# Optimization experiments

Measured on AMD Instinct MI355X. Metric: run time of the kernel, lower is better.

Reference implementation:

```python
import jax, jax.numpy as jnp
import numpy as np

NODE_DIM = 512
HIDDEN = 4096
N_NODES = 4096  # must equal HIDDEN for pool Linear to typecheck (as in source)
N_EDGES = 131072


def setup_inputs() -> dict:
    key = jax.random.key(0)
    ks = jax.random.split(key, 12)
    s1 = 0.02
    x = jax.random.normal(ks[0], (N_NODES, NODE_DIM), dtype=jnp.float32)
    edge_index = jax.random.randint(ks[1], (2, N_EDGES), 0, N_NODES, dtype=jnp.int64)
    # encoder: Linear(node_dim, hidden) -> ReLU -> Linear(hidden, hidden)
    W1 = jax.random.normal(ks[2], (NODE_DIM, HIDDEN), dtype=jnp.float32) * s1
    b1 = jnp.zeros((HIDDEN,), dtype=jnp.float32)
    W2 = jax.random.normal(ks[3], (HIDDEN, HIDDEN), dtype=jnp.float32) * s1
    b2 = jnp.zeros((HIDDEN,), dtype=jnp.float32)
    # pool: Linear(hidden, hidden) -> ReLU -> Linear(hidden, 1)
    W3 = jax.random.normal(ks[4], (HIDDEN, HIDDEN), dtype=jnp.float32) * s1
    b3 = jnp.zeros((HIDDEN,), dtype=jnp.float32)
    W4 = jax.random.normal(ks[5], (HIDDEN, 1), dtype=jnp.float32) * s1
    b4 = jnp.zeros((1,), dtype=jnp.float32)
    return {"x": x, "edge_index": edge_index, "W1": W1, "b1": b1,
            "W2": W2, "b2": b2, "W3": W3, "b3": b3, "W4": W4, "b4": b4}


def reference(x, edge_index, W1, b1, W2, b2, W3, b3, W4, b4):
    # encoder MLP: [N, node_dim] -> [N, hidden]
    h = jax.nn.relu(x @ W1 + b1) @ W2 + b2
    # kernel_vector = (h @ h.T).sum(1) == h @ h.sum(0)  (avoids O(N^2) Gram)
    s = h.sum(axis=0)                 # [hidden]
    kernel_vector = h @ s             # [N]
    kv = kernel_vector[None, :]       # [1, N] with N == hidden
    pooled = jax.nn.relu(kv @ W3 + b3) @ W4 + b4   # [1, 1]
    return pooled
```

## Files before the change

kernel.cpp:

```cpp
#include <hip/hip_runtime.h>

#define NODES 4096
#define NDIM  512
#define HID   4096

typedef __attribute__((ext_vector_type(8))) short bf16x8;
typedef __attribute__((ext_vector_type(4))) float f32x4;

__device__ __forceinline__ float b2f(short v) {
  union { unsigned int u; float f; } c;
  c.u = ((unsigned int)(unsigned short)v) << 16;
  return c.f;
}
__device__ __forceinline__ short f2b(float f) {
  union { float f; unsigned int u; } c; c.f = f;
  unsigned int r = c.u + 0x7fffu + ((c.u >> 16) & 1u);
  return (short)(r >> 16);
}

__global__ __launch_bounds__(256) void k_prep(const float* __restrict__ x,
                                              const float* __restrict__ W1,
                                              const float* __restrict__ b2,
                                              const float* __restrict__ b3,
                                              short* __restrict__ xb,
                                              short* __restrict__ w1t,
                                              float* __restrict__ aacc,
                                              float* __restrict__ svec,
                                              float* __restrict__ uacc) {
  __shared__ float tile[32][33];
  int b = blockIdx.x;
  if (b < 2048) {
    int i = (b * 256 + threadIdx.x) * 4;
    float4 v = *(const float4*)(x + i);
    short4 o;
    o.x = f2b(v.x); o.y = f2b(v.y); o.z = f2b(v.z); o.w = f2b(v.w);
    *(short4*)(xb + i) = o;
  } else if (b < 4096) {
    int t = b - 2048;
    int n0 = (t & 127) * 32;
    int k0 = (t >> 7) * 32;
    int tx = threadIdx.x & 31, ty = threadIdx.x >> 5;
    #pragma unroll
    for (int j = 0; j < 4; ++j) {
      int kk = ty + j * 8;
      tile[kk][tx] = W1[(size_t)(k0 + kk) * HID + n0 + tx];
    }
    __syncthreads();
    #pragma unroll
    for (int j = 0; j < 4; ++j) {
      int nn = ty + j * 8;
      w1t[(size_t)(n0 + nn) * NDIM + k0 + tx] = f2b(tile[tx][nn]);
    }
  } else {
    int j = (b - 4096) * 256 + threadIdx.x;
    aacc[j] = 0.0f;
    svec[j] = (float)NODES * b2[j];
    uacc[j] = b3[j];
  }
}

__global__ __launch_bounds__(512, 2) void k_gemm1(const short* __restrict__ xb,
                                                  const short* __restrict__ w1t,
                                                  const float* __restrict__ b1,
                                                  short* __restrict__ Aout,
                                                  float* __restrict__ colsum) {
  extern __shared__ char smem[];
  __shared__ float csum[256];

  const int tid  = threadIdx.x;
  const int lane = tid & 63;
  const int wid  = tid >> 6;
  const int wr   = wid >> 2;
  const int wc   = wid & 3;

  int bswz = (blockIdx.x & 7) * 32 + (blockIdx.x >> 3);
  const int brow = (bswz >> 4) * 256, bcol = (bswz & 15) * 256;

  f32x4 acc[8][4];
  #pragma unroll
  for (int i = 0; i < 8; ++i)
    #pragma unroll
    for (int j = 0; j < 4; ++j)
      acc[i][j] = (f32x4){0.f, 0.f, 0.f, 0.f};

  if (tid < 256) csum[tid] = 0.f;

  const int fr = lane & 15;
  const int fk = (lane >> 4) * 8;

  const int off0 = tid * 16;
  const int row0 = off0 >> 6, ce0 = (off0 & 63) >> 1;
  const short* gA0 = xb  + (size_t)(brow + row0) * NDIM + ce0;
  const short* gA1 = xb  + (size_t)(brow + row0 + 128) * NDIM + ce0;
  const short* gB0 = w1t + (size_t)(bcol + row0) * NDIM + ce0;
  const short* gB1 = w1t + (size_t)(bcol + row0 + 128) * NDIM + ce0;

  auto STAGE = [&](int buf, int kt2) {
    char* baseA = smem + buf * 32768;
    char* baseB = smem + 65536 + buf * 32768;
    const int ks = kt2 * 64;
    #pragma unroll
    for (int kh = 0; kh < 2; ++kh) {
      __builtin_amdgcn_global_load_lds(
          (const __attribute__((address_space(1))) void*)(gA0 + ks + kh * 32),
          (__attribute__((address_space(3))) void*)(baseA + kh * 16384 + off0), 16, 0, 0);
      __builtin_amdgcn_global_load_lds(
          (const __attribute__((address_space(1))) void*)(gA1 + ks + kh * 32),
          (__attribute__((address_space(3))) void*)(baseA + kh * 16384 + off0 + 8192), 16, 0, 0);
      __builtin_amdgcn_global_load_lds(
          (const __attribute__((address_space(1))) void*)(gB0 + ks + kh * 32),
          (__attribute__((address_space(3))) void*)(baseB + kh * 16384 + off0), 16, 0, 0);
      __builtin_amdgcn_global_load_lds(
          (const __attribute__((address_space(1))) void*)(gB1 + ks + kh * 32),
          (__attribute__((address_space(3))) void*)(baseB + kh * 16384 + off0 + 8192), 16, 0, 0);
    }
  };

  auto COMPUTE = [&](int buf) {
    #pragma unroll
    for (int kh = 0; kh < 2; ++kh) {
      bf16x8 af[8], bfr[4];
      const short* Ab = (const short*)(smem + buf * 32768 + kh * 16384);
      const short* Bb = (const short*)(smem + 65536 + buf * 32768 + kh * 16384);
      #pragma unroll
      for (int ni = 0; ni < 4; ++ni)
        bfr[ni] = *(const bf16x8*)(Bb + (wc * 64 + ni * 16 + fr) * 32 + fk);
      #pragma unroll
      for (int mi = 0; mi < 8; ++mi)
        af[mi] = *(const bf16x8*)(Ab + (wr * 128 + mi * 16 + fr) * 32 + fk);
      __builtin_amdgcn_s_setprio(1);
      #pragma unroll
      for (int mi = 0; mi < 8; ++mi)
        #pragma unroll
        for (int ni = 0; ni < 4; ++ni)
          acc[mi][ni] = __builtin_amdgcn_mfma_f32_16x16x32_bf16(bfr[ni], af[mi],
                                                                acc[mi][ni], 0, 0, 0);
      __builtin_amdgcn_s_setprio(0);
    }
  };

  STAGE(0, 0);
  #pragma unroll 1
  for (int kt2 = 0; kt2 < NDIM / 64 - 1; ++kt2) {
    STAGE((kt2 + 1) & 1, kt2 + 1);
    asm volatile("s_waitcnt vmcnt(8)" ::: "memory");
    __builtin_amdgcn_s_barrier();
    COMPUTE(kt2 & 1);
    __builtin_amdgcn_s_barrier();
  }
  asm volatile("s_waitcnt vmcnt(0)" ::: "memory");
  __builtin_amdgcn_s_barrier();
  COMPUTE((NDIM / 64 - 1) & 1);

  const int cr = lane & 15;
  const int cg = (lane >> 4) * 4;
  float4 bias4[4];
  #pragma unroll
  for (int ni = 0; ni < 4; ++ni)
    bias4[ni] = *(const float4*)(b1 + bcol + wc * 64 + ni * 16 + cg);

  float cl[4][4];
  #pragma unroll
  for (int ni = 0; ni < 4; ++ni)
    #pragma unroll
    for (int r = 0; r < 4; ++r)
      cl[ni][r] = 0.f;

  #pragma unroll
  for (int mi = 0; mi < 8; ++mi) {
    int grow = brow + wr * 128 + mi * 16 + cr;
    short* orow = Aout + (size_t)grow * HID + bcol + wc * 64;
    #pragma unroll
    for (int ni = 0; ni < 4; ++ni) {
      float v0 = fmaxf(acc[mi][ni][0] + bias4[ni].x, 0.f);
      float v1 = fmaxf(acc[mi][ni][1] + bias4[ni].y, 0.f);
      float v2 = fmaxf(acc[mi][ni][2] + bias4[ni].z, 0.f);
      float v3 = fmaxf(acc[mi][ni][3] + bias4[ni].w, 0.f);
      cl[ni][0] += v0; cl[ni][1] += v1; cl[ni][2] += v2; cl[ni][3] += v3;
      short4 o;
      o.x = f2b(v0); o.y = f2b(v1); o.z = f2b(v2); o.w = f2b(v3);
      *(short4*)(orow + ni * 16 + cg) = o;
    }
  }
  #pragma unroll
  for (int ni = 0; ni < 4; ++ni)
    #pragma unroll
    for (int r = 0; r < 4; ++r) {
      #pragma unroll
      for (int m = 1; m < 16; m <<= 1)
        cl[ni][r] += __shfl_xor(cl[ni][r], m);
    }
  if (cr == 0) {
    #pragma unroll
    for (int ni = 0; ni < 4; ++ni)
      #pragma unroll
      for (int r = 0; r < 4; ++r)
        atomicAdd(&csum[wc * 64 + ni * 16 + cg + r], cl[ni][r]);
  }
  __syncthreads();
  if (tid < 256) atomicAdd(&colsum[bcol + tid], csum[tid]);
}

__global__ __launch_bounds__(256) void k_gemv_at(const float* __restrict__ W,
                                                 const float* __restrict__ vin,
                                                 float* __restrict__ vout) {
  const int col = blockIdx.x * 1024 + threadIdx.x * 4;
  const int r0  = blockIdx.y * 64;
  float4 accv = {0.f, 0.f, 0.f, 0.f};
  const float* base = W + (size_t)r0 * HID + col;
  #pragma unroll 16
  for (int i = 0; i < 64; ++i) {
    float vi = vin[r0 + i];
    float4 wv = *(const float4*)(base + (size_t)i * HID);
    accv.x += vi * wv.x; accv.y += vi * wv.y;
    accv.z += vi * wv.z; accv.w += vi * wv.w;
  }
  atomicAdd(&vout[col + 0], accv.x);
  atomicAdd(&vout[col + 1], accv.y);
  atomicAdd(&vout[col + 2], accv.z);
  atomicAdd(&vout[col + 3], accv.w);
}

__global__ __launch_bounds__(256) void k_gemv_row(const float* __restrict__ W,
                                                  const float* __restrict__ vin,
                                                  const float* __restrict__ b2,
                                                  float* __restrict__ vout,
                                                  float* __restrict__ beta) {
  __shared__ float red[4];
  if (blockIdx.x == HID / 4) {
    float p = 0.f;
    for (int j = threadIdx.x; j < HID; j += 256) p += b2[j] * vin[j];
    #pragma unroll
    for (int o = 32; o > 0; o >>= 1) p += __shfl_down(p, o);
    int lane = threadIdx.x & 63, w = threadIdx.x >> 6;
    if (lane == 0) red[w] = p;
    __syncthreads();
    if (threadIdx.x == 0) beta[0] = red[0] + red[1] + red[2] + red[3];
    return;
  }
  int w = threadIdx.x >> 6, lane = threadIdx.x & 63;
  int row = blockIdx.x * 4 + w;
  const float* base = W + (size_t)row * HID;
  float p = 0.f;
  #pragma unroll 8
  for (int j = lane * 4; j < HID; j += 256) {
    float4 wv = *(const float4*)(base + j);
    float4 sv = *(const float4*)(vin + j);
    p += wv.x * sv.x + wv.y * sv.y + wv.z * sv.z + wv.w * sv.w;
  }
  #pragma unroll
  for (int o = 32; o > 0; o >>= 1) p += __shfl_down(p, o);
  if (lane == 0) vout[row] = p;
}

__global__ __launch_bounds__(256) void k_kv(const short* __restrict__ A,
                                            const float* __restrict__ t,
                                            const float* __restrict__ beta,
                                            float* __restrict__ kv) {
  int w = threadIdx.x >> 6, lane = threadIdx.x & 63;
  int row = blockIdx.x * 4 + w;
  const short* base = A + (size_t)row * HID;
  float p = 0.f;
  #pragma unroll
  for (int j = lane * 8; j < HID; j += 512) {
    bf16x8 av = *(const bf16x8*)(base + j);
    float4 t0 = *(const float4*)(t + j);
    float4 t1 = *(const float4*)(t + j + 4);
    p += b2f(av[0]) * t0.x + b2f(av[1]) * t0.y + b2f(av[2]) * t0.z + b2f(av[3]) * t0.w
       + b2f(av[4]) * t1.x + b2f(av[5]) * t1.y + b2f(av[6]) * t1.z + b2f(av[7]) * t1.w;
  }
  #pragma unroll
  for (int o = 32; o > 0; o >>= 1) p += __shfl_down(p, o);
  if (lane == 0) kv[row] = p + beta[0];
}

__global__ __launch_bounds__(256) void k_final(const float* __restrict__ uacc,
                                               const float* __restrict__ W4,
                                               const float* __restrict__ b4,
                                               float* __restrict__ out) {
  __shared__ float red[4];
  float p = 0.f;
  for (int j = threadIdx.x; j < HID; j += 256) {
    float uv = uacc[j];
    uv = uv > 0.f ? uv : 0.f;
    p += uv * W4[j];
  }
  #pragma unroll
  for (int o = 32; o > 0; o >>= 1) p += __shfl_down(p, o);
  int lane = threadIdx.x & 63, w = threadIdx.x >> 6;
  if (lane == 0) red[w] = p;
  __syncthreads();
  if (threadIdx.x == 0) out[0] = red[0] + red[1] + red[2] + red[3] + b4[0];
}

extern "C" void kernel_launch(void* const* d_in, const int* in_sizes, int n_in,
                              void* d_out, int out_size, void* d_ws, size_t ws_size,
                              hipStream_t stream) {
  const float* x  = (const float*)d_in[0];
  const float* W1 = (const float*)d_in[2];
  const float* b1 = (const float*)d_in[3];
  const float* W2 = (const float*)d_in[4];
  const float* b2 = (const float*)d_in[5];
  const float* W3 = (const float*)d_in[6];
  const float* b3 = (const float*)d_in[7];
  const float* W4 = (const float*)d_in[8];
  const float* b4 = (const float*)d_in[9];
  float* out = (float*)d_out;

  char* ws = (char*)d_ws;
  short* Abf  = (short*)(ws);
  short* xb   = (short*)(ws + 33554432);
  short* w1t  = (short*)(ws + 37748736);
  float* aacc = (float*)(ws + 41943040);
  float* svec = (float*)(ws + 41959424);
  float* tvec = (float*)(ws + 41975808);
  float* kvv  = (float*)(ws + 41992192);
  float* uacc = (float*)(ws + 42008576);
  float* beta = (float*)(ws + 42024960);

  k_prep    <<<dim3(4112),     dim3(256), 0, stream>>>(x, W1, b2, b3, xb, w1t, aacc, svec, uacc);
  k_gemm1   <<<dim3(256),      dim3(512), 131072, stream>>>(xb, w1t, b1, Abf, aacc);
  k_gemv_at <<<dim3(4, 64),    dim3(256), 0, stream>>>(W2, aacc, svec);
  k_gemv_row<<<dim3(1025),     dim3(256), 0, stream>>>(W2, svec, b2, tvec, beta);
  k_kv      <<<dim3(1024),     dim3(256), 0, stream>>>(Abf, tvec, beta, kvv);
  k_gemv_at <<<dim3(4, 64),    dim3(256), 0, stream>>>(W3, kvv, uacc);
  k_final   <<<dim3(1),        dim3(256), 0, stream>>>(uacc, W4, b4, out);
}
```

Measured before the change: 96.32 us.

## Swizzle LDS operand layout and stage GEMM1 epilogue through LDS for wide stores

Applies an XOR swizzle to the k-chunk placement of A/B tiles in LDS, both on the global-to-LDS load side and the fragment read side, to reduce LDS bank conflicts during MFMA operand loads. The bias/ReLU/bf16 epilogue now writes into a padded LDS tile in two halves, then all threads copy rows out with 16-byte coalesced global stores instead of scattered 8-byte stores. The epilogue adds extra barriers and reuses the operand LDS region.

```diff
diff --git a/kernel.cpp b/kernel.cpp
--- a/kernel.cpp
+++ b/kernel.cpp
@@ -86,10 +86,12 @@
   if (tid < 256) csum[tid] = 0.f;
 
   const int fr = lane & 15;
-  const int fk = (lane >> 4) * 8;
+  const int fko = ((lane >> 4) ^ ((lane >> 1) & 3)) * 8;
 
   const int off0 = tid * 16;
-  const int row0 = off0 >> 6, ce0 = (off0 & 63) >> 1;
+  const int row0 = off0 >> 6;
+  const int gs   = (off0 >> 4) & 3;
+  const int ce0  = (gs ^ ((row0 >> 1) & 3)) * 8;
   const short* gA0 = xb  + (size_t)(brow + row0) * NDIM + ce0;
   const short* gA1 = xb  + (size_t)(brow + row0 + 128) * NDIM + ce0;
   const short* gB0 = w1t + (size_t)(bcol + row0) * NDIM + ce0;
@@ -124,10 +126,10 @@
       const short* Bb = (const short*)(smem + 65536 + buf * 32768 + kh * 16384);
       #pragma unroll
       for (int ni = 0; ni < 4; ++ni)
-        bfr[ni] = *(const bf16x8*)(Bb + (wc * 64 + ni * 16 + fr) * 32 + fk);
+        bfr[ni] = *(const bf16x8*)(Bb + (wc * 64 + ni * 16 + fr) * 32 + fko);
       #pragma unroll
       for (int mi = 0; mi < 8; ++mi)
-        af[mi] = *(const bf16x8*)(Ab + (wr * 128 + mi * 16 + fr) * 32 + fk);
+        af[mi] = *(const bf16x8*)(Ab + (wr * 128 + mi * 16 + fr) * 32 + fko);
       __builtin_amdgcn_s_setprio(1);
       #pragma unroll
       for (int mi = 0; mi < 8; ++mi)
@@ -166,22 +168,37 @@
     for (int r = 0; r < 4; ++r)
       cl[ni][r] = 0.f;
 
-  #pragma unroll
-  for (int mi = 0; mi < 8; ++mi) {
-    int grow = brow + wr * 128 + mi * 16 + cr;
-    short* orow = Aout + (size_t)grow * HID + bcol + wc * 64;
-    #pragma unroll
-    for (int ni = 0; ni < 4; ++ni) {
-      float v0 = fmaxf(acc[mi][ni][0] + bias4[ni].x, 0.f);
-      float v1 = fmaxf(acc[mi][ni][1] + bias4[ni].y, 0.f);
-      float v2 = fmaxf(acc[mi][ni][2] + bias4[ni].z, 0.f);
-      float v3 = fmaxf(acc[mi][ni][3] + bias4[ni].w, 0.f);
-      cl[ni][0] += v0; cl[ni][1] += v1; cl[ni][2] += v2; cl[ni][3] += v3;
-      short4 o;
-      o.x = f2b(v0); o.y = f2b(v1); o.z = f2b(v2); o.w = f2b(v3);
-      *(short4*)(orow + ni * 16 + cg) = o;
-    }
-  }
+  short* pk = (short*)smem;
+  #pragma unroll 1
+  for (int half = 0; half < 2; ++half) {
+    __syncthreads();
+    if (wr == half) {
+      #pragma unroll
+      for (int mi = 0; mi < 8; ++mi) {
+        int lrow = mi * 16 + cr;
+        #pragma unroll
+        for (int ni = 0; ni < 4; ++ni) {
+          float v0 = fmaxf(acc[mi][ni][0] + bias4[ni].x, 0.f);
+          float v1 = fmaxf(acc[mi][ni][1] + bias4[ni].y, 0.f);
+          float v2 = fmaxf(acc[mi][ni][2] + bias4[ni].z, 0.f);
+          float v3 = fmaxf(acc[mi][ni][3] + bias4[ni].w, 0.f);
+          cl[ni][0] += v0; cl[ni][1] += v1; cl[ni][2] += v2; cl[ni][3] += v3;
+          short4 o;
+          o.x = f2b(v0); o.y = f2b(v1); o.z = f2b(v2); o.w = f2b(v3);
+          *(short4*)(pk + lrow * 264 + wc * 64 + ni * 16 + cg) = o;
+        }
+      }
+    }
+    __syncthreads();
+    #pragma unroll
+    for (int i = 0; i < 8; ++i) {
+      int c = tid + i * 512;
+      int row = c >> 5, ch = c & 31;
+      bf16x8 vv = *(const bf16x8*)(pk + row * 264 + ch * 8);
+      *(bf16x8*)(Aout + (size_t)(brow + half * 128 + row) * HID + bcol + ch * 8) = vv;
+    }
+  }
+
   #pragma unroll
   for (int ni = 0; ni < 4; ++ni)
     #pragma unroll
```

New measurement: 95.09 us. Within noise of the previous version (-1.3%).
